# Performance work log

Measured on AMD Instinct MI355X. Metric: run time of the kernel, lower is better.

Reference implementation:

```python
import jax, jax.numpy as jnp
import numpy as np

NUM_CHANNELS = 32
NUM_KNOTS = 10
GRID_RANGE = (-1.0, 1.0)


def setup_inputs() -> dict:
    key = jax.random.key(0)
    k_x, k_w = jax.random.split(key)
    x = jax.random.normal(k_x, (2, NUM_CHANNELS, 64, 64, 64), dtype=jnp.float32)
    knots = jnp.linspace(GRID_RANGE[0], GRID_RANGE[1], NUM_KNOTS, dtype=jnp.float32)
    weights = jax.random.normal(k_w, (NUM_CHANNELS, NUM_KNOTS), dtype=jnp.float32)
    return {"x": x, "knots": knots, "weights": weights}


def reference(x, knots, weights):
    # basis[b,c,d,h,w,k] = relu(x[b,c,d,h,w] - knots[k])**3
    basis = jnp.maximum(x[..., None] - knots, 0.0) ** 3  # [B,C,D,H,W,K]
    # weighted sum over knots, per channel
    return jnp.einsum('bcdhwk,ck->bcdhw', basis, weights)
```

## Files before the change

kernel.cpp:

```cpp
#include <hip/hip_runtime.h>


#define NK 10
#define CH_SHIFT 16
#define CH_MASK 31

__global__ __launch_bounds__(256) void bspline3d_kernel(
    const float* __restrict__ x,
    const float* __restrict__ knots,
    const float* __restrict__ weights,
    float* __restrict__ out,
    int nvec)
{
    float kn[NK];
#pragma unroll
    for (int k = 0; k < NK; ++k) kn[k] = knots[k];

    const int stride = gridDim.x * blockDim.x;
    for (int v = blockIdx.x * blockDim.x + threadIdx.x; v < nvec; v += stride) {
        const int c = (v >> CH_SHIFT) & CH_MASK;
        const float* __restrict__ wc = weights + c * NK;

        const float4 xv = reinterpret_cast<const float4*>(x)[v];

        float a0 = 0.f, a1 = 0.f, a2 = 0.f, a3 = 0.f;
#pragma unroll
        for (int k = 0; k < NK; ++k) {
            const float kk = kn[k];
            const float w  = wc[k];
            float b0 = fmaxf(xv.x - kk, 0.f);
            float b1 = fmaxf(xv.y - kk, 0.f);
            float b2 = fmaxf(xv.z - kk, 0.f);
            float b3 = fmaxf(xv.w - kk, 0.f);
            a0 = fmaf((b0 * b0) * b0, w, a0);
            a1 = fmaf((b1 * b1) * b1, w, a1);
            a2 = fmaf((b2 * b2) * b2, w, a2);
            a3 = fmaf((b3 * b3) * b3, w, a3);
        }
        reinterpret_cast<float4*>(out)[v] = make_float4(a0, a1, a2, a3);
    }
}

extern "C" void kernel_launch(void* const* d_in, const int* in_sizes, int n_in,
                              void* d_out, int out_size, void* d_ws, size_t ws_size,
                              hipStream_t stream) {
    const float* x       = (const float*)d_in[0];
    const float* knots   = (const float*)d_in[1];
    const float* weights = (const float*)d_in[2];
    float* out           = (float*)d_out;

    const int nvec = out_size / 4;
    const int block = 256;
    int grid = (nvec + block - 1) / block;
    if (grid > 2048) grid = 2048;

    bspline3d_kernel<<<grid, block, 0, stream>>>(x, knots, weights, out, nvec);
}
```

Before: 27.52 us.

## Assign each block a contiguous single-channel range and hoist per-channel weights

Replaces the grid-stride loop with a fixed mapping in which each block handles 2048 contiguous float4 vectors inside one channel chunk. Every block then works on a single channel, so the knot weights are loaded into registers once per block instead of once per loop iteration. The grid grows from 2048 blocks to 2048 blocks of 8 iterations each, computed from the problem size, and the inner loop is unrolled by two to keep more loads in flight. The kernel now assumes the total size is a multiple of 65536 vectors and the layout has exactly 32 channels, and it has no tail handling.

```diff
diff --git a/kernel.cpp b/kernel.cpp
--- a/kernel.cpp
+++ b/kernel.cpp
@@ -2,42 +2,51 @@
 
 
 #define NK 10
-#define CH_SHIFT 16
-#define CH_MASK 31
+#define VECS_PER_CHUNK 65536
+#define BLOCKS_PER_CHUNK 32
+#define VECS_PER_BLOCK 2048
+#define ITERS 8
 
 __global__ __launch_bounds__(256) void bspline3d_kernel(
     const float* __restrict__ x,
     const float* __restrict__ knots,
     const float* __restrict__ weights,
-    float* __restrict__ out,
-    int nvec)
+    float* __restrict__ out)
 {
-    float kn[NK];
+    const int blk   = blockIdx.x;
+    const int chunk = blk >> 5;
+    const int sub   = blk & 31;
+    const int c     = chunk & 31;
+
+    float kn[NK], w[NK];
+    const float* __restrict__ wc = weights + c * NK;
 #pragma unroll
-    for (int k = 0; k < NK; ++k) kn[k] = knots[k];
+    for (int k = 0; k < NK; ++k) { kn[k] = knots[k]; w[k] = wc[k]; }
 
-    const int stride = gridDim.x * blockDim.x;
-    for (int v = blockIdx.x * blockDim.x + threadIdx.x; v < nvec; v += stride) {
-        const int c = (v >> CH_SHIFT) & CH_MASK;
-        const float* __restrict__ wc = weights + c * NK;
+    const long base = (long)chunk * VECS_PER_CHUNK + (long)sub * VECS_PER_BLOCK;
+    const float4* __restrict__ xv4 = reinterpret_cast<const float4*>(x) + base;
+    float4* __restrict__ ov4       = reinterpret_cast<float4*>(out) + base;
 
-        const float4 xv = reinterpret_cast<const float4*>(x)[v];
+#pragma unroll 2
+    for (int i = 0; i < ITERS; ++i) {
+        const int idx = i * 256 + (int)threadIdx.x;
+        const float4 xv = xv4[idx];
 
         float a0 = 0.f, a1 = 0.f, a2 = 0.f, a3 = 0.f;
 #pragma unroll
         for (int k = 0; k < NK; ++k) {
             const float kk = kn[k];
-            const float w  = wc[k];
+            const float wk = w[k];
             float b0 = fmaxf(xv.x - kk, 0.f);
             float b1 = fmaxf(xv.y - kk, 0.f);
             float b2 = fmaxf(xv.z - kk, 0.f);
             float b3 = fmaxf(xv.w - kk, 0.f);
-            a0 = fmaf((b0 * b0) * b0, w, a0);
-            a1 = fmaf((b1 * b1) * b1, w, a1);
-            a2 = fmaf((b2 * b2) * b2, w, a2);
-            a3 = fmaf((b3 * b3) * b3, w, a3);
+            a0 = fmaf((b0 * b0) * b0, wk, a0);
+            a1 = fmaf((b1 * b1) * b1, wk, a1);
+            a2 = fmaf((b2 * b2) * b2, wk, a2);
+            a3 = fmaf((b3 * b3) * b3, wk, a3);
         }
-        reinterpret_cast<float4*>(out)[v] = make_float4(a0, a1, a2, a3);
+        ov4[idx] = make_float4(a0, a1, a2, a3);
     }
 }
 
@@ -49,10 +58,8 @@
     const float* weights = (const float*)d_in[2];
     float* out           = (float*)d_out;
 
-    const int nvec = out_size / 4;
-    const int block = 256;
-    int grid = (nvec + block - 1) / block;
-    if (grid > 2048) grid = 2048;
+    const int nchunks = (out_size / 4) / VECS_PER_CHUNK;
+    const int grid = nchunks * BLOCKS_PER_CHUNK;
 
-    bspline3d_kernel<<<grid, block, 0, stream>>>(x, knots, weights, out, nvec);
+    bspline3d_kernel<<<grid, 256, 0, stream>>>(x, knots, weights, out);
 }
```

Measured after the change: 26.39 us. 4.1% less time.
